# Kernel tuning notes

Measured on AMD Instinct MI355X. Metric: run time of the kernel, lower is better.

## Reference

```python
import jax, jax.numpy as jnp
import numpy as np

B, S, H = 2, 2048, 2048
NH, KVH, HD = 16, 4, 128
THETA = 10000.0


def setup_inputs() -> dict:
    key = jax.random.key(0)
    k1, k2, k3, k4, k5 = jax.random.split(key, 5)
    scale = 1.0 / np.sqrt(H)
    return {
        "hidden_states": jax.random.normal(k1, (B, S, H), dtype=jnp.float32),
        "Wq": jax.random.normal(k2, (H, NH * HD), dtype=jnp.float32) * scale,
        "Wk": jax.random.normal(k3, (H, KVH * HD), dtype=jnp.float32) * scale,
        "Wv": jax.random.normal(k4, (H, KVH * HD), dtype=jnp.float32) * scale,
        "Wo": jax.random.normal(k5, (NH * HD, H), dtype=jnp.float32) * scale,
    }


def _rotate_half(x):
    x1, x2 = x[..., : HD // 2], x[..., HD // 2 :]
    return jnp.concatenate((-x2, x1), axis=-1)


def _rope_cos_sin(seq_len):
    # inv_freq: [HD/2]
    inv_freq = 1.0 / (THETA ** (jnp.arange(0, HD, 2, dtype=jnp.float32) / HD))
    pos = jnp.arange(seq_len, dtype=jnp.float32)
    freqs = pos[:, None] * inv_freq[None, :]          # [S, HD/2]
    emb = jnp.concatenate((freqs, freqs), axis=-1)    # [S, HD]
    return jnp.cos(emb), jnp.sin(emb)


def reference(hidden_states, Wq, Wk, Wv, Wo):
    b, s, _ = hidden_states.shape
    n_rep = NH // KVH

    # projections -> [B, S, heads, HD]
    q = (hidden_states @ Wq).reshape(b, s, NH, HD)
    k = (hidden_states @ Wk).reshape(b, s, KVH, HD)
    v = (hidden_states @ Wv).reshape(b, s, KVH, HD)

    # RoPE (cos/sin broadcast over head dim, matching cos.unsqueeze(-2))
    cos, sin = _rope_cos_sin(s)
    cos = cos[None, :, None, :]  # [1, S, 1, HD]
    sin = sin[None, :, None, :]
    q = q * cos + _rotate_half(q) * sin
    k = k * cos + _rotate_half(k) * sin

    # repeat_kv: [B, S, KVH, HD] -> [B, S, NH, HD]
    k = jnp.repeat(k, n_rep, axis=2)
    v = jnp.repeat(v, n_rep, axis=2)

    # causal SDPA
    scores = jnp.einsum("bqhd,bkhd->bhqk", q, k) / jnp.sqrt(jnp.float32(HD))
    causal = jnp.tril(jnp.ones((s, s), dtype=bool))
    scores = jnp.where(causal[None, None], scores, jnp.finfo(scores.dtype).min)
    probs = jax.nn.softmax(scores, axis=-1)
    ctx = jnp.einsum("bhqk,bkhd->bqhd", probs, v)     # [B, S, NH, HD]

    out = ctx.reshape(b, s, NH * HD) @ Wo             # [B, S, H]
    return out
```

## Files before the change

kernel.cpp:

```cpp
#include <hip/hip_runtime.h>
#include <stdint.h>
#include <math.h>

#define BB 2
#define SS 2048
#define HH 2048
#define NH 16
#define KVH 4
#define HD 128
#define BSZ (BB*SS)
#define QW (NH*HD)
#define KVW (KVH*HD)

typedef __attribute__((ext_vector_type(8))) short s16x8;
typedef __attribute__((ext_vector_type(4))) float f32x4;

typedef const unsigned int __attribute__((address_space(1)))* gas_ptr;
typedef unsigned int __attribute__((address_space(3)))* las_ptr;

__device__ __forceinline__ unsigned short f2b(float x) {
    unsigned u = __builtin_bit_cast(unsigned, x);
    unsigned r = u + 0x7fffu + ((u >> 16) & 1u);
    return (unsigned short)(r >> 16);
}
__device__ __forceinline__ float b2f(unsigned short h) {
    unsigned u = ((unsigned)h) << 16;
    return __builtin_bit_cast(float, u);
}

__device__ __forceinline__ void gload_lds16(const void* g, void* l) {
    __builtin_amdgcn_global_load_lds((gas_ptr)g, (las_ptr)l, 16, 0, 0);
}

__device__ __forceinline__ void mfma_gemm_tile(
    const unsigned short* __restrict__ A,
    const unsigned short* __restrict__ Bt,
    int m0, int c0, f32x4 acc[4][4],
    unsigned short* As, unsigned short* Bs)
{
    const int tid  = threadIdx.x;
    const int lane = tid & 63, wave = tid >> 6;
    const int quad = lane >> 4, l15 = lane & 15;
    const int mh = wave >> 1, nh = wave & 1;
    const int srow = lane >> 2;
    const int sk   = (lane & 3) * 8;

#pragma unroll
    for (int i = 0; i < 4; ++i)
#pragma unroll
        for (int j = 0; j < 4; ++j) acc[i][j] = (f32x4){0.f, 0.f, 0.f, 0.f};

    for (int k0 = 0; k0 < HH; k0 += 32) {
        __syncthreads();
#pragma unroll
        for (int j = 0; j < 2; ++j) {
            int chunk = wave * 2 + j;
            int row = chunk * 16 + srow;
            gload_lds16(A  + (size_t)(m0 + row) * HH + k0 + sk, As + chunk * 512);
            gload_lds16(Bt + (size_t)(c0 + row) * HH + k0 + sk, Bs + chunk * 512);
        }
        __syncthreads();

        s16x8 af[4], bf[4];
#pragma unroll
        for (int t = 0; t < 4; ++t) {
            af[t] = *(const s16x8*)(As + (mh * 64 + t * 16 + l15) * 32 + quad * 8);
            bf[t] = *(const s16x8*)(Bs + (nh * 64 + t * 16 + l15) * 32 + quad * 8);
        }
#pragma unroll
        for (int mt = 0; mt < 4; ++mt)
#pragma unroll
            for (int nt = 0; nt < 4; ++nt)
                acc[mt][nt] = __builtin_amdgcn_mfma_f32_16x16x32_bf16(
                    af[mt], bf[nt], acc[mt][nt], 0, 0, 0);
    }
}

__global__ __launch_bounds__(256) void gemm_qkv(
    const unsigned short* __restrict__ Ah,
    const unsigned short* __restrict__ Wqt,
    const unsigned short* __restrict__ Wkt,
    const unsigned short* __restrict__ Wvt,
    unsigned short* __restrict__ Qb,
    unsigned short* __restrict__ Kb,
    unsigned short* __restrict__ Vb)
{
    __shared__ __align__(16) unsigned short As[128 * 32];
    __shared__ __align__(16) unsigned short Bs[128 * 32];
    const int nblk = blockIdx.x * 128;
    const int m0 = blockIdx.y * 128;
    const unsigned short* Bt;
    unsigned short* C;
    int c0, ldc;
    if (nblk < QW)            { Bt = Wqt; C = Qb; c0 = nblk;            ldc = QW;  }
    else if (nblk < QW + KVW) { Bt = Wkt; C = Kb; c0 = nblk - QW;       ldc = KVW; }
    else                      { Bt = Wvt; C = Vb; c0 = nblk - QW - KVW; ldc = KVW; }

    f32x4 acc[4][4];
    mfma_gemm_tile(Ah, Bt, m0, c0, acc, As, Bs);

    const int lane = threadIdx.x & 63, wave = threadIdx.x >> 6;
    const int quad = lane >> 4, l15 = lane & 15;
    const int mh = wave >> 1, nh = wave & 1;
#pragma unroll
    for (int mt = 0; mt < 4; ++mt)
#pragma unroll
        for (int nt = 0; nt < 4; ++nt)
#pragma unroll
            for (int r = 0; r < 4; ++r) {
                int row = m0 + mh * 64 + mt * 16 + quad * 4 + r;
                int col = c0 + nh * 64 + nt * 16 + l15;
                C[(size_t)row * ldc + col] = f2b(acc[mt][nt][r]);
            }
}

__global__ __launch_bounds__(256) void gemm_out(
    const unsigned short* __restrict__ ctx,
    const unsigned short* __restrict__ Wot,
    float* __restrict__ out)
{
    __shared__ __align__(16) unsigned short As[128 * 32];
    __shared__ __align__(16) unsigned short Bs[128 * 32];
    const int c0 = blockIdx.x * 128;
    const int m0 = blockIdx.y * 128;

    f32x4 acc[4][4];
    mfma_gemm_tile(ctx, Wot, m0, c0, acc, As, Bs);

    const int lane = threadIdx.x & 63, wave = threadIdx.x >> 6;
    const int quad = lane >> 4, l15 = lane & 15;
    const int mh = wave >> 1, nh = wave & 1;
#pragma unroll
    for (int mt = 0; mt < 4; ++mt)
#pragma unroll
        for (int nt = 0; nt < 4; ++nt)
#pragma unroll
            for (int r = 0; r < 4; ++r) {
                int row = m0 + mh * 64 + mt * 16 + quad * 4 + r;
                int col = c0 + nh * 64 + nt * 16 + l15;
                out[(size_t)row * HH + col] = acc[mt][nt][r];
            }
}

__global__ __launch_bounds__(256) void convert_bf16(const float* __restrict__ in,
                                                    unsigned short* __restrict__ out,
                                                    int n)
{
    int i = (blockIdx.x * 256 + threadIdx.x) * 4;
    if (i >= n) return;
    float4 v = *(const float4*)(in + i);
    ushort4 o = make_ushort4(f2b(v.x), f2b(v.y), f2b(v.z), f2b(v.w));
    *(ushort4*)(out + i) = o;
}

__global__ __launch_bounds__(256) void transpose_all(
    const float* __restrict__ Wq, const float* __restrict__ Wk,
    const float* __restrict__ Wv, const float* __restrict__ Wo,
    unsigned short* __restrict__ Wqt, unsigned short* __restrict__ Wkt,
    unsigned short* __restrict__ Wvt, unsigned short* __restrict__ Wot)
{
    const int z = blockIdx.z;
    const float* in;
    unsigned short* out;
    int N;
    if (z == 0)      { in = Wq; out = Wqt; N = QW;  }
    else if (z == 1) { in = Wk; out = Wkt; N = KVW; }
    else if (z == 2) { in = Wv; out = Wvt; N = KVW; }
    else             { in = Wo; out = Wot; N = HH;  }
    const int n0 = blockIdx.x * 32;
    if (n0 >= N) return;
    const int k0 = blockIdx.y * 32;

    __shared__ float t[32][33];
    const int c = threadIdx.x & 31, r = threadIdx.x >> 5;
#pragma unroll
    for (int j = 0; j < 4; ++j)
        t[r + j * 8][c] = in[(size_t)(k0 + r + j * 8) * N + n0 + c];
    __syncthreads();
#pragma unroll
    for (int j = 0; j < 4; ++j)
        out[(size_t)(n0 + r + j * 8) * HH + k0 + c] = f2b(t[c][r + j * 8]);
}

__global__ __launch_bounds__(256) void vtrans_bf16(const unsigned short* __restrict__ Vb,
                                                   unsigned short* __restrict__ Vtg)
{
    __shared__ unsigned short t[32][33];
    const int s0 = blockIdx.x * 32, c0 = blockIdx.y * 32, b = blockIdx.z;
    const int cc = threadIdx.x & 31, r = threadIdx.x >> 5;
#pragma unroll
    for (int j = 0; j < 4; ++j)
        t[r + j * 8][cc] = Vb[(size_t)(b * SS + s0 + r + j * 8) * KVW + c0 + cc];
    __syncthreads();
#pragma unroll
    for (int j = 0; j < 4; ++j)
        Vtg[(size_t)(b * KVW + c0 + r + j * 8) * SS + s0 + cc] = t[cc][r + j * 8];
}

__global__ __launch_bounds__(256) void rope_all(unsigned short* __restrict__ Qb,
                                                unsigned short* __restrict__ Kb)
{
    int idx = blockIdx.x * 256 + threadIdx.x;
    const int totalQ = BSZ * NH * 64;
    unsigned short* X;
    int nheads; float mul;
    if (idx < totalQ) { X = Qb; nheads = NH; mul = 0.08838834764831845f; }
    else              { X = Kb; nheads = KVH; mul = 1.0f; idx -= totalQ; }
    int j = idx & 63;
    int t = idx >> 6;
    int hh = t % nheads;
    int bs = t / nheads;
    int s = bs & (SS - 1);
    float inv = exp2f(-0.2076205063f * (float)j);
    float ang = (float)s * inv;
    float c = __cosf(ang), sn = __sinf(ang);
    size_t base = (size_t)bs * ((size_t)nheads * HD) + (size_t)hh * HD;
    float x1 = b2f(X[base + j]);
    float x2 = b2f(X[base + j + 64]);
    X[base + j]      = f2b((x1 * c - x2 * sn) * mul);
    X[base + j + 64] = f2b((x2 * c + x1 * sn) * mul);
}

__global__ __launch_bounds__(256) void attn_mfma(
    const unsigned short* __restrict__ Qb,
    const unsigned short* __restrict__ Kb,
    const unsigned short* __restrict__ Vtg,
    unsigned short* __restrict__ ctx)
{
    const int b   = blockIdx.x;
    const int h   = blockIdx.y;
    const int qtp = 15 - blockIdx.z;
    const int kvh = h >> 2;
    const int q0  = qtp * 128;
    const int tid = threadIdx.x;
    const int lane = tid & 63, wave = tid >> 6;
    const int quad = lane >> 4, l15 = lane & 15;

    __shared__ __align__(16) unsigned short Ks[64 * 128];
    __shared__ __align__(16) unsigned short Vt[128 * 64];
    __shared__ __align__(16) unsigned short Ps[4][32 * 72];

    const int krb = tid >> 4;
    const int c8k = tid & 15;
    const int dv  = tid >> 3;
    const int c8v = tid & 7;

    const unsigned short* Kbase = Kb  + (size_t)b * SS * KVW + kvh * HD;
    const unsigned short* Vbase = Vtg + (size_t)(b * KVW + kvh * HD) * SS;

    s16x8 qf[2][4];
#pragma unroll
    for (int rt = 0; rt < 2; ++rt) {
        const unsigned short* qrow =
            Qb + (size_t)(b * SS + q0 + wave * 32 + rt * 16 + l15) * QW + h * HD;
#pragma unroll
        for (int dc = 0; dc < 4; ++dc)
            qf[rt][dc] = *(const s16x8*)(qrow + dc * 32 + quad * 8);
    }

    f32x4 oacc[2][8];
#pragma unroll
    for (int rt = 0; rt < 2; ++rt)
#pragma unroll
        for (int i = 0; i < 8; ++i) oacc[rt][i] = (f32x4){0.f, 0.f, 0.f, 0.f};
    f32x4 lacc[2] = {(f32x4){0.f,0.f,0.f,0.f}, (f32x4){0.f,0.f,0.f,0.f}};

    const s16x8 vone = {0x3F80, 0x3F80, 0x3F80, 0x3F80,
                        0x3F80, 0x3F80, 0x3F80, 0x3F80};

    s16x8 kpre[4], vpre[4];
#pragma unroll
    for (int u = 0; u < 4; ++u) {
        kpre[u] = *(const s16x8*)(Kbase + (size_t)(u * 16 + krb) * KVW + c8k * 8);
        vpre[u] = *(const s16x8*)(Vbase + (size_t)(u * 32 + dv) * SS + c8v * 8);
    }

    const int nkt = 2 * qtp + 2;
    for (int kt = 0; kt < nkt; ++kt) {
        const int k0 = kt * 64;
        __syncthreads();

#pragma unroll
        for (int u = 0; u < 4; ++u) {
            *(s16x8*)(Ks + (u * 16 + krb) * 128 + ((c8k ^ krb) * 8)) = kpre[u];
            *(s16x8*)(Vt + (u * 32 + dv) * 64 + ((c8v ^ (dv & 7)) * 8)) = vpre[u];
        }
        __syncthreads();

        if (kt + 1 < nkt) {
            const int kn = k0 + 64;
#pragma unroll
            for (int u = 0; u < 4; ++u) {
                kpre[u] = *(const s16x8*)(Kbase + (size_t)(kn + u * 16 + krb) * KVW + c8k * 8);
                vpre[u] = *(const s16x8*)(Vbase + (size_t)(u * 32 + dv) * SS + kn + c8v * 8);
            }
        }

        f32x4 sc[2][4];
#pragma unroll
        for (int rt = 0; rt < 2; ++rt)
#pragma unroll
            for (int tk = 0; tk < 4; ++tk) sc[rt][tk] = (f32x4){0.f, 0.f, 0.f, 0.f};
#pragma unroll
        for (int tk = 0; tk < 4; ++tk) {
#pragma unroll
            for (int dc = 0; dc < 4; ++dc) {
                s16x8 kf = *(const s16x8*)(Ks + (tk * 16 + l15) * 128
                                              + (((dc * 4 + quad) ^ l15) * 8));
                sc[0][tk] = __builtin_amdgcn_mfma_f32_16x16x32_bf16(qf[0][dc], kf, sc[0][tk], 0, 0, 0);
                sc[1][tk] = __builtin_amdgcn_mfma_f32_16x16x32_bf16(qf[1][dc], kf, sc[1][tk], 0, 0, 0);
            }
        }

        unsigned short* pw = &Ps[wave][0];
#pragma unroll
        for (int rt = 0; rt < 2; ++rt) {
            const int rowbase = q0 + wave * 32 + rt * 16;
            const bool straddle = (k0 + 63 > rowbase);
#pragma unroll
            for (int tk = 0; tk < 4; ++tk) {
                const int col = k0 + tk * 16 + l15;
#pragma unroll
                for (int r = 0; r < 4; ++r) {
                    float p = __expf(sc[rt][tk][r] - 10.0f);
                    if (straddle && col > rowbase + quad * 4 + r) p = 0.f;
                    pw[(rt * 16 + quad * 4 + r) * 72 + tk * 16 + l15] = f2b(p);
                }
            }
        }

        s16x8 pf[2][2];
#pragma unroll
        for (int rt = 0; rt < 2; ++rt)
#pragma unroll
            for (int kc = 0; kc < 2; ++kc)
                pf[rt][kc] = *(const s16x8*)(pw + (rt * 16 + l15) * 72
                                             + kc * 32 + quad * 8);
#pragma unroll
        for (int rt = 0; rt < 2; ++rt)
#pragma unroll
            for (int kc = 0; kc < 2; ++kc)
                lacc[rt] = __builtin_amdgcn_mfma_f32_16x16x32_bf16(pf[rt][kc], vone, lacc[rt], 0, 0, 0);
#pragma unroll
        for (int dt = 0; dt < 8; ++dt) {
#pragma unroll
            for (int kc = 0; kc < 2; ++kc) {
                s16x8 vf = *(const s16x8*)(Vt + (dt * 16 + l15) * 64
                                              + (((kc * 4 + quad) ^ (l15 & 7)) * 8));
                oacc[0][dt] = __builtin_amdgcn_mfma_f32_16x16x32_bf16(pf[0][kc], vf, oacc[0][dt], 0, 0, 0);
                oacc[1][dt] = __builtin_amdgcn_mfma_f32_16x16x32_bf16(pf[1][kc], vf, oacc[1][dt], 0, 0, 0);
            }
        }
    }

#pragma unroll
    for (int rt = 0; rt < 2; ++rt) {
        float linv[4];
#pragma unroll
        for (int r = 0; r < 4; ++r) linv[r] = 1.0f / lacc[rt][r];
#pragma unroll
        for (int dt = 0; dt < 8; ++dt)
#pragma unroll
            for (int r = 0; r < 4; ++r) {
                int row = b * SS + q0 + wave * 32 + rt * 16 + quad * 4 + r;
                ctx[(size_t)row * QW + h * HD + dt * 16 + l15] =
                    f2b(oacc[rt][dt][r] * linv[r]);
            }
    }
}

extern "C" void kernel_launch(void* const* d_in, const int* in_sizes, int n_in,
                              void* d_out, int out_size, void* d_ws, size_t ws_size,
                              hipStream_t stream)
{
    const float* hidden = (const float*)d_in[0];
    const float* Wq = (const float*)d_in[1];
    const float* Wk = (const float*)d_in[2];
    const float* Wv = (const float*)d_in[3];
    const float* Wo = (const float*)d_in[4];
    float* out = (float*)d_out;

    unsigned short* Ah  = (unsigned short*)d_ws;
    unsigned short* Wqt = Ah  + (size_t)BSZ * HH;
    unsigned short* Wkt = Wqt + (size_t)QW * HH;
    unsigned short* Wvt = Wkt + (size_t)KVW * HH;
    unsigned short* Wot = Wvt + (size_t)KVW * HH;
    unsigned short* Qb  = Wot + (size_t)HH * QW;
    unsigned short* Kb  = Qb  + (size_t)BSZ * QW;
    unsigned short* Vb  = Kb  + (size_t)BSZ * KVW;
    unsigned short* ctx = Vb  + (size_t)BSZ * KVW;
    unsigned short* Vtg = ctx + (size_t)BSZ * QW;

    convert_bf16<<<(BSZ * HH / 4 + 255) / 256, 256, 0, stream>>>(hidden, Ah, BSZ * HH);
    transpose_all<<<dim3(64, 64, 4), 256, 0, stream>>>(Wq, Wk, Wv, Wo,
                                                       Wqt, Wkt, Wvt, Wot);

    gemm_qkv<<<dim3((QW + 2 * KVW) / 128, BSZ / 128), 256, 0, stream>>>(
        Ah, Wqt, Wkt, Wvt, Qb, Kb, Vb);

    vtrans_bf16<<<dim3(SS / 32, KVW / 32, BB), 256, 0, stream>>>(Vb, Vtg);

    rope_all<<<(BSZ * (NH + KVH) * 64) / 256, 256, 0, stream>>>(Qb, Kb);

    attn_mfma<<<dim3(BB, NH, SS / 128), 256, 0, stream>>>(Qb, Kb, Vtg, ctx);

    gemm_out<<<dim3(HH / 128, BSZ / 128), 256, 0, stream>>>(ctx, Wot, out);
}
```

Baseline: 315.6 us.

## Share K/V tiles across GQA heads per block and fuse Q RoPE into attention

Each attention block now covers one batch, one KV head and a 32-row query tile, with its four waves handling the four query heads that share that KV head. Each K/V tile loaded into shared memory is therefore reused by four heads instead of one, and the tile grows to 128 keys with a causal early exit per 64-key half. The RoPE and scaling of Q move into the attention kernel's register prologue, so the standalone RoPE pass now touches only K. The cost is double the shared memory for the K and V tiles, more prefetch registers (launch bounds now request two blocks per CU), and more sincos work per block.

Result: no change. 318.9 us (+1.0%).

```diff
diff --git a/kernel.cpp b/kernel.cpp
--- a/kernel.cpp
+++ b/kernel.cpp
@@ -197,53 +197,46 @@
         Vtg[(size_t)(b * KVW + c0 + r + j * 8) * SS + s0 + cc] = t[cc][r + j * 8];
 }
 
-__global__ __launch_bounds__(256) void rope_all(unsigned short* __restrict__ Qb,
-                                                unsigned short* __restrict__ Kb)
+__global__ __launch_bounds__(256) void rope_k(unsigned short* __restrict__ Kb)
 {
     int idx = blockIdx.x * 256 + threadIdx.x;
-    const int totalQ = BSZ * NH * 64;
-    unsigned short* X;
-    int nheads; float mul;
-    if (idx < totalQ) { X = Qb; nheads = NH; mul = 0.08838834764831845f; }
-    else              { X = Kb; nheads = KVH; mul = 1.0f; idx -= totalQ; }
     int j = idx & 63;
     int t = idx >> 6;
-    int hh = t % nheads;
-    int bs = t / nheads;
+    int hh = t & (KVH - 1);
+    int bs = t >> 2;
     int s = bs & (SS - 1);
     float inv = exp2f(-0.2076205063f * (float)j);
     float ang = (float)s * inv;
     float c = __cosf(ang), sn = __sinf(ang);
-    size_t base = (size_t)bs * ((size_t)nheads * HD) + (size_t)hh * HD;
-    float x1 = b2f(X[base + j]);
-    float x2 = b2f(X[base + j + 64]);
-    X[base + j]      = f2b((x1 * c - x2 * sn) * mul);
-    X[base + j + 64] = f2b((x2 * c + x1 * sn) * mul);
-}
-
-__global__ __launch_bounds__(256) void attn_mfma(
+    size_t base = (size_t)bs * KVW + (size_t)hh * HD;
+    float x1 = b2f(Kb[base + j]);
+    float x2 = b2f(Kb[base + j + 64]);
+    Kb[base + j]      = f2b(x1 * c - x2 * sn);
+    Kb[base + j + 64] = f2b(x2 * c + x1 * sn);
+}
+
+__global__ __launch_bounds__(256, 2) void attn_mfma(
     const unsigned short* __restrict__ Qb,
     const unsigned short* __restrict__ Kb,
     const unsigned short* __restrict__ Vtg,
     unsigned short* __restrict__ ctx)
 {
-    const int b   = blockIdx.x;
-    const int h   = blockIdx.y;
-    const int qtp = 15 - blockIdx.z;
-    const int kvh = h >> 2;
-    const int q0  = qtp * 128;
+    const int bk  = blockIdx.x;
+    const int b   = bk >> 2, kvh = bk & 3;
+    const int p   = 63 - (int)blockIdx.y;
+    const int q0  = p * 32;
+    const int rowmax = q0 + 31;
     const int tid = threadIdx.x;
     const int lane = tid & 63, wave = tid >> 6;
+    const int h = kvh * 4 + wave;
     const int quad = lane >> 4, l15 = lane & 15;
 
-    __shared__ __align__(16) unsigned short Ks[64 * 128];
-    __shared__ __align__(16) unsigned short Vt[128 * 64];
-    __shared__ __align__(16) unsigned short Ps[4][32 * 72];
-
-    const int krb = tid >> 4;
-    const int c8k = tid & 15;
-    const int dv  = tid >> 3;
-    const int c8v = tid & 7;
+    __shared__ __align__(16) unsigned short Ks[128 * 128];
+    __shared__ __align__(16) unsigned short Vt[128 * 128];
+    __shared__ __align__(16) unsigned short Ps[4][16 * 72];
+
+    const int srow = tid >> 4;
+    const int sc8  = tid & 15;
 
     const unsigned short* Kbase = Kb  + (size_t)b * SS * KVW + kvh * HD;
     const unsigned short* Vbase = Vtg + (size_t)(b * KVW + kvh * HD) * SS;
@@ -252,11 +245,29 @@
 #pragma unroll
     for (int rt = 0; rt < 2; ++rt) {
         const unsigned short* qrow =
-            Qb + (size_t)(b * SS + q0 + wave * 32 + rt * 16 + l15) * QW + h * HD;
+            Qb + (size_t)(b * SS + q0 + rt * 16 + l15) * QW + h * HD;
 #pragma unroll
         for (int dc = 0; dc < 4; ++dc)
             qf[rt][dc] = *(const s16x8*)(qrow + dc * 32 + quad * 8);
     }
+#pragma unroll
+    for (int rt = 0; rt < 2; ++rt) {
+        const float pos = (float)(q0 + rt * 16 + l15);
+#pragma unroll
+        for (int dcp = 0; dcp < 2; ++dcp)
+#pragma unroll
+            for (int i = 0; i < 8; ++i) {
+                int jj = dcp * 32 + quad * 8 + i;
+                float inv = exp2f(-0.2076205063f * (float)jj);
+                float ang = pos * inv;
+                float sn, cs;
+                __sincosf(ang, &sn, &cs);
+                float x1 = b2f((unsigned short)qf[rt][dcp][i]);
+                float x2 = b2f((unsigned short)qf[rt][dcp + 2][i]);
+                qf[rt][dcp][i]     = (short)f2b((x1 * cs - x2 * sn) * 0.08838834764831845f);
+                qf[rt][dcp + 2][i] = (short)f2b((x2 * cs + x1 * sn) * 0.08838834764831845f);
+            }
+    }
 
     f32x4 oacc[2][8];
 #pragma unroll
@@ -268,87 +279,91 @@
     const s16x8 vone = {0x3F80, 0x3F80, 0x3F80, 0x3F80,
                         0x3F80, 0x3F80, 0x3F80, 0x3F80};
 
-    s16x8 kpre[4], vpre[4];
-#pragma unroll
-    for (int u = 0; u < 4; ++u) {
-        kpre[u] = *(const s16x8*)(Kbase + (size_t)(u * 16 + krb) * KVW + c8k * 8);
-        vpre[u] = *(const s16x8*)(Vbase + (size_t)(u * 32 + dv) * SS + c8v * 8);
-    }
-
-    const int nkt = 2 * qtp + 2;
+    s16x8 kpre[8], vpre[8];
+#pragma unroll
+    for (int u = 0; u < 8; ++u) {
+        kpre[u] = *(const s16x8*)(Kbase + (size_t)(u * 16 + srow) * KVW + sc8 * 8);
+        vpre[u] = *(const s16x8*)(Vbase + (size_t)(u * 16 + srow) * SS + sc8 * 8);
+    }
+
+    const int nkt = (p >> 2) + 1;
     for (int kt = 0; kt < nkt; ++kt) {
-        const int k0 = kt * 64;
+        const int k0 = kt * 128;
         __syncthreads();
 
 #pragma unroll
-        for (int u = 0; u < 4; ++u) {
-            *(s16x8*)(Ks + (u * 16 + krb) * 128 + ((c8k ^ krb) * 8)) = kpre[u];
-            *(s16x8*)(Vt + (u * 32 + dv) * 64 + ((c8v ^ (dv & 7)) * 8)) = vpre[u];
+        for (int u = 0; u < 8; ++u) {
+            *(s16x8*)(Ks + (u * 16 + srow) * 128 + ((sc8 ^ srow) * 8)) = kpre[u];
+            *(s16x8*)(Vt + (u * 16 + srow) * 128 + ((sc8 ^ srow) * 8)) = vpre[u];
         }
         __syncthreads();
 
         if (kt + 1 < nkt) {
-            const int kn = k0 + 64;
-#pragma unroll
-            for (int u = 0; u < 4; ++u) {
-                kpre[u] = *(const s16x8*)(Kbase + (size_t)(kn + u * 16 + krb) * KVW + c8k * 8);
-                vpre[u] = *(const s16x8*)(Vbase + (size_t)(u * 32 + dv) * SS + kn + c8v * 8);
+            const int kn = k0 + 128;
+#pragma unroll
+            for (int u = 0; u < 8; ++u) {
+                kpre[u] = *(const s16x8*)(Kbase + (size_t)(kn + u * 16 + srow) * KVW + sc8 * 8);
+                vpre[u] = *(const s16x8*)(Vbase + (size_t)(u * 16 + srow) * SS + kn + sc8 * 8);
             }
         }
 
-        f32x4 sc[2][4];
-#pragma unroll
-        for (int rt = 0; rt < 2; ++rt)
-#pragma unroll
-            for (int tk = 0; tk < 4; ++tk) sc[rt][tk] = (f32x4){0.f, 0.f, 0.f, 0.f};
-#pragma unroll
-        for (int tk = 0; tk < 4; ++tk) {
-#pragma unroll
-            for (int dc = 0; dc < 4; ++dc) {
-                s16x8 kf = *(const s16x8*)(Ks + (tk * 16 + l15) * 128
-                                              + (((dc * 4 + quad) ^ l15) * 8));
-                sc[0][tk] = __builtin_amdgcn_mfma_f32_16x16x32_bf16(qf[0][dc], kf, sc[0][tk], 0, 0, 0);
-                sc[1][tk] = __builtin_amdgcn_mfma_f32_16x16x32_bf16(qf[1][dc], kf, sc[1][tk], 0, 0, 0);
-            }
-        }
-
-        unsigned short* pw = &Ps[wave][0];
-#pragma unroll
-        for (int rt = 0; rt < 2; ++rt) {
-            const int rowbase = q0 + wave * 32 + rt * 16;
-            const bool straddle = (k0 + 63 > rowbase);
+#pragma unroll
+        for (int half = 0; half < 2; ++half) {
+            const int kh0 = k0 + half * 64;
+            if (kh0 > rowmax) break;
+
+            f32x4 sc[2][4];
+#pragma unroll
+            for (int rt = 0; rt < 2; ++rt)
+#pragma unroll
+                for (int tk = 0; tk < 4; ++tk) sc[rt][tk] = (f32x4){0.f,0.f,0.f,0.f};
 #pragma unroll
             for (int tk = 0; tk < 4; ++tk) {
-                const int col = k0 + tk * 16 + l15;
-#pragma unroll
-                for (int r = 0; r < 4; ++r) {
-                    float p = __expf(sc[rt][tk][r] - 10.0f);
-                    if (straddle && col > rowbase + quad * 4 + r) p = 0.f;
-                    pw[(rt * 16 + quad * 4 + r) * 72 + tk * 16 + l15] = f2b(p);
+#pragma unroll
+                for (int dc = 0; dc < 4; ++dc) {
+                    s16x8 kf = *(const s16x8*)(Ks + (half * 64 + tk * 16 + l15) * 128
+                                                  + (((dc * 4 + quad) ^ l15) * 8));
+                    sc[0][tk] = __builtin_amdgcn_mfma_f32_16x16x32_bf16(qf[0][dc], kf, sc[0][tk], 0, 0, 0);
+                    sc[1][tk] = __builtin_amdgcn_mfma_f32_16x16x32_bf16(qf[1][dc], kf, sc[1][tk], 0, 0, 0);
                 }
             }
-        }
-
-        s16x8 pf[2][2];
-#pragma unroll
-        for (int rt = 0; rt < 2; ++rt)
-#pragma unroll
-            for (int kc = 0; kc < 2; ++kc)
-                pf[rt][kc] = *(const s16x8*)(pw + (rt * 16 + l15) * 72
-                                             + kc * 32 + quad * 8);
-#pragma unroll
-        for (int rt = 0; rt < 2; ++rt)
-#pragma unroll
-            for (int kc = 0; kc < 2; ++kc)
-                lacc[rt] = __builtin_amdgcn_mfma_f32_16x16x32_bf16(pf[rt][kc], vone, lacc[rt], 0, 0, 0);
-#pragma unroll
-        for (int dt = 0; dt < 8; ++dt) {
-#pragma unroll
-            for (int kc = 0; kc < 2; ++kc) {
-                s16x8 vf = *(const s16x8*)(Vt + (dt * 16 + l15) * 64
-                                              + (((kc * 4 + quad) ^ (l15 & 7)) * 8));
-                oacc[0][dt] = __builtin_amdgcn_mfma_f32_16x16x32_bf16(pf[0][kc], vf, oacc[0][dt], 0, 0, 0);
-                oacc[1][dt] = __builtin_amdgcn_mfma_f32_16x16x32_bf16(pf[1][kc], vf, oacc[1][dt], 0, 0, 0);
+
+            unsigned short* pw = &Ps[wave][0];
+            s16x8 pf[2][2];
+#pragma unroll
+            for (int rt = 0; rt < 2; ++rt) {
+                const int rowbase = q0 + rt * 16;
+                const bool straddle = (kh0 + 63 > rowbase);
+#pragma unroll
+                for (int tk = 0; tk < 4; ++tk) {
+                    const int col = kh0 + tk * 16 + l15;
+#pragma unroll
+                    for (int r = 0; r < 4; ++r) {
+                        float pv = __expf(sc[rt][tk][r] - 10.0f);
+                        if (straddle && col > rowbase + quad * 4 + r) pv = 0.f;
+                        pw[(quad * 4 + r) * 72 + tk * 16 + l15] = f2b(pv);
+                    }
+                }
+#pragma unroll
+                for (int kc = 0; kc < 2; ++kc)
+                    pf[rt][kc] = *(const s16x8*)(pw + l15 * 72 + kc * 32 + quad * 8);
+            }
+
+#pragma unroll
+            for (int rt = 0; rt < 2; ++rt)
+#pragma unroll
+                for (int kc = 0; kc < 2; ++kc)
+                    lacc[rt] = __builtin_amdgcn_mfma_f32_16x16x32_bf16(pf[rt][kc], vone, lacc[rt], 0, 0, 0);
+
+#pragma unroll
+            for (int dt = 0; dt < 8; ++dt) {
+#pragma unroll
+                for (int kc = 0; kc < 2; ++kc) {
+                    s16x8 vf = *(const s16x8*)(Vt + (dt * 16 + l15) * 128
+                                                  + (((half * 8 + kc * 4 + quad) ^ l15) * 8));
+                    oacc[0][dt] = __builtin_amdgcn_mfma_f32_16x16x32_bf16(pf[0][kc], vf, oacc[0][dt], 0, 0, 0);
+                    oacc[1][dt] = __builtin_amdgcn_mfma_f32_16x16x32_bf16(pf[1][kc], vf, oacc[1][dt], 0, 0, 0);
+                }
             }
         }
     }
@@ -362,7 +377,7 @@
         for (int dt = 0; dt < 8; ++dt)
 #pragma unroll
             for (int r = 0; r < 4; ++r) {
-                int row = b * SS + q0 + wave * 32 + rt * 16 + quad * 4 + r;
+                int row = b * SS + q0 + rt * 16 + quad * 4 + r;
                 ctx[(size_t)row * QW + h * HD + dt * 16 + l15] =
                     f2b(oacc[rt][dt][r] * linv[r]);
             }
@@ -400,9 +415,9 @@
 
     vtrans_bf16<<<dim3(SS / 32, KVW / 32, BB), 256, 0, stream>>>(Vb, Vtg);
 
-    rope_all<<<(BSZ * (NH + KVH) * 64) / 256, 256, 0, stream>>>(Qb, Kb);
-
-    attn_mfma<<<dim3(BB, NH, SS / 128), 256, 0, stream>>>(Qb, Kb, Vtg, ctx);
+    rope_k<<<(BSZ * KVH * 64) / 256, 256, 0, stream>>>(Kb);
+
+    attn_mfma<<<dim3(BB * KVH, SS / 32), 256, 0, stream>>>(Qb, Kb, Vtg, ctx);
 
     gemm_out<<<dim3(HH / 128, BSZ / 128), 256, 0, stream>>>(ctx, Wot, out);
 }
```
